# Optimization experiments

Hardware: AMD Instinct MI355X
Metric: run time of the kernel (lower is better)

Reference implementation:

```python
import jax, jax.numpy as jnp
import numpy as np

ORDER = 16
FRAME = 160
EPS = 1e-8


def setup_inputs() -> dict:
    key = jax.random.key(0)
    B, T = 64, 320000  # 64 utterances x 20s @ 16kHz; T % FRAME == 0
    x = jax.random.normal(key, (B, T), dtype=jnp.float32)
    return {"x": x}


def _lpc_residual(x):
    # x: [B, T] -> residual [B, T, 1]
    B, T = x.shape
    F = T // FRAME
    frm = x.reshape(B, F, FRAME)  # [B, F, 160]

    # Autocorrelation lags 0..ORDER (equiv. np.correlate(frm, frm, 'full')[160-1 : 160+16])
    r = jnp.stack(
        [jnp.sum(frm[..., : FRAME - k] * frm[..., k:], axis=-1) for k in range(ORDER + 1)],
        axis=-1,
    )  # [B, F, 17]

    # Levinson-Durbin recursion, batched over (B, F); loop over fixed small ORDER.
    a = jnp.zeros((B, F, ORDER + 1), dtype=x.dtype).at[..., 0].set(1.0)
    e = jnp.where(r[..., 0] != 0, r[..., 0], EPS)
    for i in range(1, ORDER + 1):
        # acc = r[i] - sum_{j=1}^{i-1} a[j] * r[i-j]
        acc = r[..., i] - jnp.sum(a[..., 1:i] * r[..., 1:i][..., ::-1], axis=-1)
        safe_e = jnp.where(e != 0, e, 1.0)
        k = jnp.where(e != 0, acc / safe_e, 0.0)
        a_new = a[..., 1:i] - k[..., None] * a[..., i - 1:0:-1]
        a = a.at[..., 1:i].set(a_new)
        a = a.at[..., i].set(k)
        e = jnp.maximum(e * (1.0 - k * k), EPS)

    # FIR filter: lfilter(a, [1.0], frm) -> res[n] = sum_k a[k] * frm[n-k] (zero-padded)
    res = a[..., 0:1] * frm
    for k in range(1, ORDER + 1):
        shifted = jnp.pad(frm, ((0, 0), (0, 0), (k, 0)))[..., :FRAME]
        res = res + a[..., k:k + 1] * shifted

    return res.reshape(B, T)[..., None]


def reference(x):
    return _lpc_residual(x)
```

## Files before the change

### kernel.cpp

```cpp
#include <hip/hip_runtime.h>

#define FRAME 160
#define ORDER 16
#define LPC_EPS 1e-8f
#define NF 32
#define BS 256
#define SEG 20
#define SX 164
#define QPB (NF * FRAME / 4 / BS)

__global__ __launch_bounds__(BS, 4) void lpc_fused(const float* __restrict__ x,
                                                   float* __restrict__ out) {
    __shared__ float xs[NF * SX];

    const int t = threadIdx.x;
    const int ln = t & 63;
    const long long base = (long long)blockIdx.x * (NF * FRAME);

#pragma unroll
    for (int it = 0; it < QPB; ++it) {
        int p = it * BS + t;
        int f = p / 40;
        int off = (p - f * 40) * 4;
        float4 v = *(const float4*)(x + base + 4 * p);
        *(float4*)(&xs[f * SX + off]) = v;
    }
    __syncthreads();

    const int fi = t >> 3;
    const int part = t & 7;
    const int sbase = SEG * part;

    float w[SEG + ORDER];
#pragma unroll
    for (int m = 0; m < (SEG + ORDER) / 4; ++m) {
        int idx = sbase + 4 * m;
        float4 v = make_float4(0.f, 0.f, 0.f, 0.f);
        if (idx < FRAME) v = *(const float4*)(&xs[fi * SX + idx]);
        w[4 * m + 0] = v.x; w[4 * m + 1] = v.y;
        w[4 * m + 2] = v.z; w[4 * m + 3] = v.w;
    }

    float pre[ORDER];
#pragma unroll
    for (int m = 0; m < ORDER / 4; ++m) {
        int idx = sbase - ORDER + 4 * m;
        float4 v = make_float4(0.f, 0.f, 0.f, 0.f);
        if (idx >= 0) v = *(const float4*)(&xs[fi * SX + idx]);
        pre[4 * m + 0] = v.x; pre[4 * m + 1] = v.y;
        pre[4 * m + 2] = v.z; pre[4 * m + 3] = v.w;
    }

    float r[ORDER + 1];
#pragma unroll
    for (int k = 0; k <= ORDER; ++k) r[k] = 0.f;
#pragma unroll
    for (int n = 0; n < SEG; ++n) {
#pragma unroll
        for (int k = 0; k <= ORDER; ++k) {
            r[k] = fmaf(w[n], w[n + k], r[k]);
        }
    }
#pragma unroll
    for (int k = 0; k <= ORDER; ++k) {
        r[k] += __shfl_xor(r[k], 1);
        r[k] += __shfl_xor(r[k], 2);
        r[k] += __shfl_xor(r[k], 4);
    }

    float rr[ORDER + 1];
#pragma unroll
    for (int k = 0; k <= ORDER; ++k)
        rr[k] = __shfl(r[k], (ln & 7) << 3);

    float ao[ORDER + 1];
    ao[0] = 1.f;
#pragma unroll
    for (int j = 1; j <= ORDER; ++j) ao[j] = 0.f;
    float e = (rr[0] != 0.f) ? rr[0] : LPC_EPS;
#pragma unroll
    for (int i = 1; i <= ORDER; ++i) {
        float acc = rr[i];
#pragma unroll
        for (int j = 1; j < i; ++j) acc -= ao[j] * rr[i - j];
        float k = acc * __builtin_amdgcn_rcpf(e);
#pragma unroll
        for (int j = 1; 2 * j < i; ++j) {
            float aj = ao[j], aij = ao[i - j];
            ao[j]     = aj  - k * aij;
            ao[i - j] = aij - k * aj;
        }
        if ((i & 1) == 0) {
            int m = i >> 1;
            ao[m] = ao[m] - k * ao[m];
        }
        ao[i] = k;
        e = fmaxf(e * (1.f - k * k), LPC_EPS);
    }

    float a[ORDER + 1];
    a[0] = 1.f;
#pragma unroll
    for (int k = 1; k <= ORDER; ++k)
        a[k] = __shfl(ao[k], ln >> 3);

#pragma unroll
    for (int m = 0; m < SEG / 4; ++m) {
        float o[4];
#pragma unroll
        for (int i = 0; i < 4; ++i) {
            int n = 4 * m + i;
            float s = 0.f;
#pragma unroll
            for (int k = 0; k <= ORDER; ++k) {
                int j = n - k;
                float xv = (j >= 0) ? w[j] : pre[ORDER + j];
                s = fmaf(a[k], xv, s);
            }
            o[i] = s;
        }
        *(float4*)(&xs[fi * SX + sbase + 4 * m]) = make_float4(o[0], o[1], o[2], o[3]);
    }
    __syncthreads();

#pragma unroll
    for (int it = 0; it < QPB; ++it) {
        int p = it * BS + t;
        int f = p / 40;
        int off = (p - f * 40) * 4;
        float4 v = *(const float4*)(&xs[f * SX + off]);
        *(float4*)(out + base + 4 * p) = v;
    }
}

extern "C" void kernel_launch(void* const* d_in, const int* in_sizes, int n_in,
                              void* d_out, int out_size, void* d_ws, size_t ws_size,
                              hipStream_t stream) {
    const float* x = (const float*)d_in[0];
    float* out = (float*)d_out;
    int total = in_sizes[0];
    int n_frames = total / FRAME;
    int n_blocks = n_frames / NF;
    lpc_fused<<<n_blocks, BS, 0, stream>>>(x, out);
}
```

Baseline: 41.64 us.

## Double-buffer tiles with direct global-to-LDS loads and per-wave frame ownership

Each block now handles two 32-frame tiles and double-buffers them in LDS. It uses global_load_lds DMA so the next tile's load overlaps the current tile's compute. The layout is reorganized so each wave owns its 8 frames, which replaces block-wide syncs with a barrier plus hand-set vmcnt waits and makes the write-out per-wave. It halves the grid and doubles LDS use. The manual waitcnt counts and the padded 41-quad layout are fragile and may lower occupancy or tail parallelism.

```diff
diff --git a/kernel.cpp b/kernel.cpp
--- a/kernel.cpp
+++ b/kernel.cpp
@@ -6,130 +6,161 @@
 #define NF 32
 #define BS 256
 #define SEG 20
-#define SX 164
-#define QPB (NF * FRAME / 4 / BS)
+#define SXF 164
+#define WCH 1536
+#define TQ (NF * FRAME)
+#define T 2
+
+__device__ __forceinline__ void dma16(const float* g, float* l) {
+    __builtin_amdgcn_global_load_lds(
+        (const __attribute__((address_space(1))) void*)g,
+        (__attribute__((address_space(3))) void*)l, 16, 0, 0);
+}
 
 __global__ __launch_bounds__(BS, 4) void lpc_fused(const float* __restrict__ x,
                                                    float* __restrict__ out) {
-    __shared__ float xs[NF * SX];
+    __shared__ float xs[2][4 * WCH];
 
     const int t = threadIdx.x;
+    const int wv = t >> 6;
     const int ln = t & 63;
-    const long long base = (long long)blockIdx.x * (NF * FRAME);
-
-#pragma unroll
-    for (int it = 0; it < QPB; ++it) {
-        int p = it * BS + t;
-        int f = p / 40;
-        int off = (p - f * 40) * 4;
-        float4 v = *(const float4*)(x + base + 4 * p);
-        *(float4*)(&xs[f * SX + off]) = v;
-    }
-    __syncthreads();
+    const long long tile0 = (long long)blockIdx.x * T;
 
     const int fi = t >> 3;
     const int part = t & 7;
     const int sbase = SEG * part;
+    const int rowb = wv * WCH + (fi & 7) * SXF;
 
-    float w[SEG + ORDER];
+    auto issue = [&](int c, long long gbase) {
 #pragma unroll
-    for (int m = 0; m < (SEG + ORDER) / 4; ++m) {
-        int idx = sbase + 4 * m;
-        float4 v = make_float4(0.f, 0.f, 0.f, 0.f);
-        if (idx < FRAME) v = *(const float4*)(&xs[fi * SX + idx]);
-        w[4 * m + 0] = v.x; w[4 * m + 1] = v.y;
-        w[4 * m + 2] = v.z; w[4 * m + 3] = v.w;
-    }
+        for (int it = 0; it < 6; ++it) {
+            int ql = it * 64 + ln;
+            int fl = ql / 41;
+            int off = ql - fl * 41;
+            int rf = (fl < 8) ? fl : 7;
+            int ro = (off < 40) ? off : 39;
+            int gq = (wv * 8 + rf) * 40 + ro;
+            dma16(x + gbase + (long long)gq * 4,
+                  &xs[c][wv * WCH + it * 256]);
+        }
+    };
 
-    float pre[ORDER];
+    issue(0, tile0 * TQ);
+
 #pragma unroll
-    for (int m = 0; m < ORDER / 4; ++m) {
-        int idx = sbase - ORDER + 4 * m;
-        float4 v = make_float4(0.f, 0.f, 0.f, 0.f);
-        if (idx >= 0) v = *(const float4*)(&xs[fi * SX + idx]);
-        pre[4 * m + 0] = v.x; pre[4 * m + 1] = v.y;
-        pre[4 * m + 2] = v.z; pre[4 * m + 3] = v.w;
-    }
+    for (int tt = 0; tt < T; ++tt) {
+        const int c = tt & 1;
+        const long long gbase = (tile0 + tt) * TQ;
 
-    float r[ORDER + 1];
+        if (tt + 1 < T) issue(c ^ 1, gbase + TQ);
+        if (tt == 0)            asm volatile("s_waitcnt vmcnt(6)" ::: "memory");
+        else if (tt + 1 < T)    asm volatile("s_waitcnt vmcnt(11)" ::: "memory");
+        else                    asm volatile("s_waitcnt vmcnt(5)" ::: "memory");
+        __builtin_amdgcn_sched_barrier(0);
+        __builtin_amdgcn_s_barrier();
+
+        float w[SEG + ORDER];
 #pragma unroll
-    for (int k = 0; k <= ORDER; ++k) r[k] = 0.f;
+        for (int m = 0; m < (SEG + ORDER) / 4; ++m) {
+            int idx = sbase + 4 * m;
+            float4 v = make_float4(0.f, 0.f, 0.f, 0.f);
+            if (idx < FRAME) v = *(const float4*)(&xs[c][rowb + idx]);
+            w[4 * m + 0] = v.x; w[4 * m + 1] = v.y;
+            w[4 * m + 2] = v.z; w[4 * m + 3] = v.w;
+        }
+
+        float pre[ORDER];
 #pragma unroll
-    for (int n = 0; n < SEG; ++n) {
+        for (int m = 0; m < ORDER / 4; ++m) {
+            int idx = sbase - ORDER + 4 * m;
+            float4 v = make_float4(0.f, 0.f, 0.f, 0.f);
+            if (idx >= 0) v = *(const float4*)(&xs[c][rowb + idx]);
+            pre[4 * m + 0] = v.x; pre[4 * m + 1] = v.y;
+            pre[4 * m + 2] = v.z; pre[4 * m + 3] = v.w;
+        }
+
+        float r[ORDER + 1];
+#pragma unroll
+        for (int k = 0; k <= ORDER; ++k) r[k] = 0.f;
+#pragma unroll
+        for (int n = 0; n < SEG; ++n) {
+#pragma unroll
+            for (int k = 0; k <= ORDER; ++k) {
+                r[k] = fmaf(w[n], w[n + k], r[k]);
+            }
+        }
 #pragma unroll
         for (int k = 0; k <= ORDER; ++k) {
-            r[k] = fmaf(w[n], w[n + k], r[k]);
+            r[k] += __shfl_xor(r[k], 1);
+            r[k] += __shfl_xor(r[k], 2);
+            r[k] += __shfl_xor(r[k], 4);
         }
-    }
+
+        float rr[ORDER + 1];
 #pragma unroll
-    for (int k = 0; k <= ORDER; ++k) {
-        r[k] += __shfl_xor(r[k], 1);
-        r[k] += __shfl_xor(r[k], 2);
-        r[k] += __shfl_xor(r[k], 4);
-    }
+        for (int k = 0; k <= ORDER; ++k)
+            rr[k] = __shfl(r[k], (ln & 7) << 3);
 
-    float rr[ORDER + 1];
+        float ao[ORDER + 1];
+        ao[0] = 1.f;
 #pragma unroll
-    for (int k = 0; k <= ORDER; ++k)
-        rr[k] = __shfl(r[k], (ln & 7) << 3);
+        for (int j = 1; j <= ORDER; ++j) ao[j] = 0.f;
+        float e = (rr[0] != 0.f) ? rr[0] : LPC_EPS;
+#pragma unroll
+        for (int i = 1; i <= ORDER; ++i) {
+            float acc = rr[i];
+#pragma unroll
+            for (int j = 1; j < i; ++j) acc -= ao[j] * rr[i - j];
+            float k = acc * __builtin_amdgcn_rcpf(e);
+#pragma unroll
+            for (int j = 1; 2 * j < i; ++j) {
+                float aj = ao[j], aij = ao[i - j];
+                ao[j]     = aj  - k * aij;
+                ao[i - j] = aij - k * aj;
+            }
+            if ((i & 1) == 0) {
+                int m = i >> 1;
+                ao[m] = ao[m] - k * ao[m];
+            }
+            ao[i] = k;
+            e = fmaxf(e * (1.f - k * k), LPC_EPS);
+        }
 
-    float ao[ORDER + 1];
-    ao[0] = 1.f;
+        float a[ORDER + 1];
+        a[0] = 1.f;
 #pragma unroll
-    for (int j = 1; j <= ORDER; ++j) ao[j] = 0.f;
-    float e = (rr[0] != 0.f) ? rr[0] : LPC_EPS;
-#pragma unroll
-    for (int i = 1; i <= ORDER; ++i) {
-        float acc = rr[i];
-#pragma unroll
-        for (int j = 1; j < i; ++j) acc -= ao[j] * rr[i - j];
-        float k = acc * __builtin_amdgcn_rcpf(e);
-#pragma unroll
-        for (int j = 1; 2 * j < i; ++j) {
-            float aj = ao[j], aij = ao[i - j];
-            ao[j]     = aj  - k * aij;
-            ao[i - j] = aij - k * aj;
-        }
-        if ((i & 1) == 0) {
-            int m = i >> 1;
-            ao[m] = ao[m] - k * ao[m];
-        }
-        ao[i] = k;
-        e = fmaxf(e * (1.f - k * k), LPC_EPS);
-    }
-
-    float a[ORDER + 1];
-    a[0] = 1.f;
-#pragma unroll
-    for (int k = 1; k <= ORDER; ++k)
-        a[k] = __shfl(ao[k], ln >> 3);
+        for (int k = 1; k <= ORDER; ++k)
+            a[k] = __shfl(ao[k], ln >> 3);
 
 #pragma unroll
-    for (int m = 0; m < SEG / 4; ++m) {
-        float o[4];
+        for (int m = 0; m < SEG / 4; ++m) {
+            float o[4];
 #pragma unroll
-        for (int i = 0; i < 4; ++i) {
-            int n = 4 * m + i;
-            float s = 0.f;
+            for (int i = 0; i < 4; ++i) {
+                int n = 4 * m + i;
+                float s = 0.f;
 #pragma unroll
-            for (int k = 0; k <= ORDER; ++k) {
-                int j = n - k;
-                float xv = (j >= 0) ? w[j] : pre[ORDER + j];
-                s = fmaf(a[k], xv, s);
+                for (int k = 0; k <= ORDER; ++k) {
+                    int j = n - k;
+                    float xv = (j >= 0) ? w[j] : pre[ORDER + j];
+                    s = fmaf(a[k], xv, s);
+                }
+                o[i] = s;
             }
-            o[i] = s;
+            *(float4*)(&xs[c][rowb + sbase + 4 * m]) =
+                make_float4(o[0], o[1], o[2], o[3]);
         }
-        *(float4*)(&xs[fi * SX + sbase + 4 * m]) = make_float4(o[0], o[1], o[2], o[3]);
-    }
-    __syncthreads();
+        asm volatile("s_waitcnt lgkmcnt(0)" ::: "memory");
+        __builtin_amdgcn_sched_barrier(0);
 
 #pragma unroll
-    for (int it = 0; it < QPB; ++it) {
-        int p = it * BS + t;
-        int f = p / 40;
-        int off = (p - f * 40) * 4;
-        float4 v = *(const float4*)(&xs[f * SX + off]);
-        *(float4*)(out + base + 4 * p) = v;
+        for (int it = 0; it < 5; ++it) {
+            int ql = it * 64 + ln;
+            int fl = ql / 40;
+            int off4 = (ql - fl * 40) * 4;
+            float4 v = *(const float4*)(&xs[c][wv * WCH + fl * SXF + off4]);
+            *(float4*)(out + gbase + (long long)(wv * 320 + ql) * 4) = v;
+        }
     }
 }
 
@@ -140,6 +171,6 @@
     float* out = (float*)d_out;
     int total = in_sizes[0];
     int n_frames = total / FRAME;
-    int n_blocks = n_frames / NF;
+    int n_blocks = n_frames / NF / T;
     lpc_fused<<<n_blocks, BS, 0, stream>>>(x, out);
 }
```

After: 47.13 us. 13.2% more time.
